# Performance work log

Hardware: AMD Instinct MI355X
Metric: run time of the kernel (lower is better)

## Reference

```python
import jax, jax.numpy as jnp
import numpy as np

B, T, DIM, NH = 2, 2048, 1024, 16
HD = DIM // NH  # 64


def setup_inputs() -> dict:
    key = jax.random.key(0)
    ks = jax.random.split(key, 5)
    x = jax.random.normal(ks[0], (B, T, DIM), dtype=jnp.float32)
    # realistic RoPE tables (any float tables work; use true rotary angles)
    inv_freq = 1.0 / (10000.0 ** (jnp.arange(0, HD, 2, dtype=jnp.float32) / HD))  # [HD/2]
    ang = jnp.arange(T, dtype=jnp.float32)[:, None] * inv_freq[None, :]           # [T, HD/2]
    ang = jnp.repeat(ang, 2, axis=-1)                                             # [T, HD] interleaved pairs
    sin = jnp.sin(ang)[None, None]  # [1,1,T,HD]
    cos = jnp.cos(ang)[None, None]
    W_qkv = jax.random.normal(ks[1], (DIM, 3 * DIM), dtype=jnp.float32) * (DIM ** -0.5)
    W_proj = jax.random.normal(ks[2], (DIM, DIM), dtype=jnp.float32) * (DIM ** -0.5)
    return {"x": x, "sin": sin, "cos": cos, "W_qkv": W_qkv, "W_proj": W_proj}


def _rope(x, sin, cos):
    # x: [B,H,T,D]; sin/cos: [1,1,T,D]
    x1, x2 = x[..., ::2], x[..., 1::2]
    xr = jnp.stack((-x2, x1), axis=-1).reshape(x.shape)  # interleave (-x2, x1)
    return x * cos + xr * sin


def reference(x, sin, cos, W_qkv, W_proj):
    Bx, Tx, C = x.shape
    nh, hd = NH, C // NH
    qkv = x @ W_qkv                                   # [B,T,3C]
    q, k, v = jnp.split(qkv, 3, axis=-1)
    to_bhtd = lambda t: t.reshape(Bx, Tx, nh, hd).transpose(0, 2, 1, 3)
    q, k, v = to_bhtd(q), to_bhtd(k), to_bhtd(v)      # [B,H,T,D]
    q = _rope(q, sin[:, :, :Tx], cos[:, :, :Tx])
    k = _rope(k, sin[:, :, :Tx], cos[:, :, :Tx])
    scale = 1.0 / jnp.sqrt(jnp.asarray(hd, dtype=x.dtype))
    scores = jnp.einsum('bhqd,bhkd->bhqk', q, k) * scale
    causal = jnp.tril(jnp.ones((Tx, Tx), dtype=bool))
    scores = jnp.where(causal, scores, jnp.finfo(scores.dtype).min)
    attn = jax.nn.softmax(scores, axis=-1)
    y = jnp.einsum('bhqk,bhkd->bhqd', attn, v)        # [B,H,T,D]
    y = y.transpose(0, 2, 1, 3).reshape(Bx, Tx, C)
    return y @ W_proj
```

## Files before the change

### kernel.cpp

```cpp
#include <hip/hip_runtime.h>


typedef float  f32x4  __attribute__((ext_vector_type(4)));
typedef __bf16 bf16x8 __attribute__((ext_vector_type(8)));
typedef short  short8 __attribute__((ext_vector_type(8)));

#define Bb   2
#define Tt   2048
#define DIMc 1024
#define NHh  16
#define HDd  64

__device__ __forceinline__ short f2bf(float f) {
    unsigned u = __builtin_bit_cast(unsigned, f);
    u += 0x7fffu + ((u >> 16) & 1u);
    return (short)(u >> 16);
}

__device__ __forceinline__ f32x4 mfma16(short8 a, short8 b, f32x4 c) {
    return __builtin_amdgcn_mfma_f32_16x16x32_bf16(
        __builtin_bit_cast(bf16x8, a), __builtin_bit_cast(bf16x8, b), c, 0, 0, 0);
}

__device__ __forceinline__ void gl_lds16(const void* g, void* l) {
    __builtin_amdgcn_global_load_lds(
        (const __attribute__((address_space(1))) unsigned int*)g,
        (__attribute__((address_space(3))) unsigned int*)l, 16, 0, 0);
}

__global__ __launch_bounds__(256) void convX(const float* __restrict__ X,
                                             short* __restrict__ Xb)
{
    size_t i = ((size_t)blockIdx.x * 256 + threadIdx.x) * 8;
    float4 a = *(const float4*)(X + i);
    float4 b = *(const float4*)(X + i + 4);
    short8 s;
    s[0] = f2bf(a.x); s[1] = f2bf(a.y); s[2] = f2bf(a.z); s[3] = f2bf(a.w);
    s[4] = f2bf(b.x); s[5] = f2bf(b.y); s[6] = f2bf(b.z); s[7] = f2bf(b.w);
    *(short8*)(Xb + i) = s;
}

__global__ __launch_bounds__(256) void convT(const float* __restrict__ W,
                                             short* __restrict__ Wt, int N)
{
    __shared__ float L[64][65];
    const int kb = blockIdx.x * 64, nb = blockIdx.y * 64;
    const int tid = threadIdx.x;
#pragma unroll
    for (int it = 0; it < 4; it++) {
        int kk = it * 16 + (tid >> 4), c = (tid & 15) * 4;
        float4 v = *(const float4*)(W + (size_t)(kb + kk) * N + nb + c);
        L[c + 0][kk] = v.x; L[c + 1][kk] = v.y;
        L[c + 2][kk] = v.z; L[c + 3][kk] = v.w;
    }
    __syncthreads();
#pragma unroll
    for (int it = 0; it < 2; it++) {
        int n = it * 32 + (tid >> 3), ks = (tid & 7) * 8;
        short8 s;
#pragma unroll
        for (int j = 0; j < 8; j++) s[j] = f2bf(L[n][ks + j]);
        *(short8*)(Wt + (size_t)(nb + n) * 1024 + kb + ks) = s;
    }
}

__global__ __launch_bounds__(256) void qkv_rope(
    const short* __restrict__ A, const short* __restrict__ Bt,
    const float* __restrict__ Sn, const float* __restrict__ Cs,
    short* __restrict__ Qo, short* __restrict__ Ko, short* __restrict__ Vt)
{
    __shared__ __align__(16) short As[128][32];
    __shared__ __align__(16) short Bs[128][32];
    const int bm = blockIdx.x, bn = blockIdx.y;
    const int tid = threadIdx.x;
    const int wv = tid >> 6, lane = tid & 63, g = lane >> 4, l16 = lane & 15;
    const int wr = wv >> 1, wc = wv & 1;

    f32x4 acc[4][4];
#pragma unroll
    for (int i = 0; i < 4; i++)
#pragma unroll
        for (int j = 0; j < 4; j++) acc[i][j] = (f32x4){0.f, 0.f, 0.f, 0.f};

    const int rA = tid >> 2, cA = (tid & 3) << 3;
    for (int k0 = 0; k0 < 1024; k0 += 32) {
#pragma unroll
        for (int i = 0; i < 2; i++)
            gl_lds16(A + (size_t)(bm * 128 + i * 64 + rA) * 1024 + k0 + cA,
                     &As[i * 64 + rA][cA]);
#pragma unroll
        for (int i = 0; i < 2; i++)
            gl_lds16(Bt + (size_t)(bn * 128 + i * 64 + rA) * 1024 + k0 + cA,
                     &Bs[i * 64 + rA][cA]);
        __syncthreads();
        short8 af[4], bfr[4];
#pragma unroll
        for (int mt = 0; mt < 4; mt++) af[mt]  = *(const short8*)&As[wr * 64 + mt * 16 + l16][g * 8];
#pragma unroll
        for (int nt = 0; nt < 4; nt++) bfr[nt] = *(const short8*)&Bs[wc * 64 + nt * 16 + l16][g * 8];
#pragma unroll
        for (int mt = 0; mt < 4; mt++)
#pragma unroll
            for (int nt = 0; nt < 4; nt++) acc[mt][nt] = mfma16(af[mt], bfr[nt], acc[mt][nt]);
        __syncthreads();
    }

#pragma unroll
    for (int mt = 0; mt < 4; mt++)
#pragma unroll
        for (int nt = 0; nt < 4; nt++)
#pragma unroll
            for (int r = 0; r < 4; r++) {
                int m = bm * 128 + wr * 64 + mt * 16 + g * 4 + r;
                int n = bn * 128 + wc * 64 + nt * 16 + l16;
                float val = acc[mt][nt][r];
                float partner = __shfl_xor(val, 1, 64);
                int b = m >> 11, t = m & 2047;
                int sec = n >> 10, nn = n & 1023;
                int h = nn >> 6, d = nn & 63;
                if (sec == 2) {
                    Vt[(((size_t)(b * 16 + h) * 64 + d) << 11) + t] = f2bf(val);
                } else {
                    float sv = Sn[t * 64 + d], cv = Cs[t * 64 + d];
                    float ro = (d & 1) ? fmaf(val, cv, partner * sv)
                                       : fmaf(val, cv, -partner * sv);
                    short* dst = (sec == 0) ? Qo : Ko;
                    dst[(((size_t)(b * 16 + h) << 11) + t) * 64 + d] = f2bf(ro);
                }
            }
}

__global__ __launch_bounds__(256, 4) void attn(
    const short* __restrict__ Q, const short* __restrict__ K,
    const short* __restrict__ V, short* __restrict__ Y)
{
    __shared__ __align__(16) short Ks[2][64][64];
    __shared__ __align__(16) short Vs[2][64][64];
    __shared__ __align__(16) short Pl[4][16][64];

    const int id = blockIdx.y * gridDim.x + blockIdx.x;
    const int bh = id >> 5;
    const int qi = ((id & 31) + ((id >> 8) << 3)) & 31;
    const int tid = threadIdx.x, wv = tid >> 6, lane = tid & 63;
    const int g = lane >> 4, l16 = lane & 15;
    const int q0w = qi * 64 + wv * 16;
    const short* Qb = Q + (size_t)bh * Tt * 64;
    const short* Kb = K + (size_t)bh * Tt * 64;
    const short* Vb = V + (size_t)bh * 64 * Tt;

    const int rj = lane >> 3, cc = lane & 7, gc = cc ^ rj;

    auto stage = [&](int s, int buf) {
        int k0s = s * 64;
#pragma unroll
        for (int j = 0; j < 2; j++) {
            int row = wv * 16 + j * 8 + rj;
            gl_lds16(Kb + (size_t)(k0s + row) * 64 + gc * 8, &Ks[buf][row][cc << 3]);
        }
#pragma unroll
        for (int j = 0; j < 2; j++) {
            int row = wv * 16 + j * 8 + rj;
            gl_lds16(Vb + (size_t)row * Tt + k0s + gc * 8, &Vs[buf][row][cc << 3]);
        }
    };

    short8 qf[2];
#pragma unroll
    for (int ss = 0; ss < 2; ss++)
        qf[ss] = *(const short8*)(Qb + (size_t)(q0w + l16) * 64 + ss * 32 + g * 8);

    f32x4 o[4];
#pragma unroll
    for (int nt = 0; nt < 4; nt++) o[nt] = (f32x4){0.f, 0.f, 0.f, 0.f};
    float lsum[4] = {0.f, 0.f, 0.f, 0.f};

    const int nsteps = qi + 1;
    const int sw = l16 & 7;

    stage(0, 0);
    __syncthreads();

    for (int s = 0; s < nsteps; ++s) {
        if (s + 1 < nsteps) stage(s + 1, (s + 1) & 1);
        const int kb = s & 1, k0 = s * 64;

        f32x4 S[4];
#pragma unroll
        for (int t = 0; t < 4; t++) {
            S[t] = (f32x4){0.f, 0.f, 0.f, 0.f};
#pragma unroll
            for (int ss = 0; ss < 2; ss++) {
                short8 kf = *(const short8*)&Ks[kb][t * 16 + l16][((ss * 4 + g) ^ sw) << 3];
                S[t] = mfma16(qf[ss], kf, S[t]);
            }
        }

        float p[4][4];
        if (s < nsteps - 1) {
#pragma unroll
            for (int t = 0; t < 4; t++)
#pragma unroll
                for (int r = 0; r < 4; r++)
                    p[t][r] = __expf(fmaf(S[t][r], 0.125f, -10.f));
        } else {
#pragma unroll
            for (int t = 0; t < 4; t++)
#pragma unroll
                for (int r = 0; r < 4; r++) {
                    int key = k0 + t * 16 + l16, qq = q0w + g * 4 + r;
                    p[t][r] = (key <= qq) ? __expf(fmaf(S[t][r], 0.125f, -10.f)) : 0.f;
                }
        }
#pragma unroll
        for (int r = 0; r < 4; r++)
            lsum[r] += (p[0][r] + p[1][r]) + (p[2][r] + p[3][r]);

#pragma unroll
        for (int t = 0; t < 4; t++)
#pragma unroll
            for (int r = 0; r < 4; r++) {
                int row = g * 4 + r, c = t * 16 + l16;
                Pl[wv][row][(((c >> 3) ^ (row & 7)) << 3) | (c & 7)] = f2bf(p[t][r]);
            }
        asm volatile("" ::: "memory");
        short8 pf[2];
#pragma unroll
        for (int ks = 0; ks < 2; ks++)
            pf[ks] = *(const short8*)&Pl[wv][l16][((ks * 4 + g) ^ sw) << 3];
#pragma unroll
        for (int nt = 0; nt < 4; nt++)
#pragma unroll
            for (int ks = 0; ks < 2; ks++) {
                short8 vf = *(const short8*)&Vs[kb][nt * 16 + l16][((ks * 4 + g) ^ sw) << 3];
                o[nt] = mfma16(pf[ks], vf, o[nt]);
            }
        __syncthreads();
    }

    float inv[4];
#pragma unroll
    for (int r = 0; r < 4; r++) {
        float t = lsum[r];
        t += __shfl_xor(t, 1, 64);
        t += __shfl_xor(t, 2, 64);
        t += __shfl_xor(t, 4, 64);
        t += __shfl_xor(t, 8, 64);
        inv[r] = 1.0f / t;
    }
    const int b = bh >> 4, h = bh & 15;
#pragma unroll
    for (int nt = 0; nt < 4; nt++)
#pragma unroll
        for (int r = 0; r < 4; r++) {
            int qq = q0w + g * 4 + r, d = nt * 16 + l16;
            Y[((size_t)(b * Tt + qq)) * DIMc + h * 64 + d] = f2bf(o[nt][r] * inv[r]);
        }
}

__global__ __launch_bounds__(256) void proj(
    const short* __restrict__ A, const short* __restrict__ Bt, float* __restrict__ O)
{
    __shared__ __align__(16) short As[128][32];
    __shared__ __align__(16) short Bs[128][32];
    const int bm = blockIdx.x, bn = blockIdx.y;
    const int tid = threadIdx.x;
    const int wv = tid >> 6, lane = tid & 63, g = lane >> 4, l16 = lane & 15;
    const int wr = wv >> 1, wc = wv & 1;

    f32x4 acc[4][4];
#pragma unroll
    for (int i = 0; i < 4; i++)
#pragma unroll
        for (int j = 0; j < 4; j++) acc[i][j] = (f32x4){0.f, 0.f, 0.f, 0.f};

    const int rA = tid >> 2, cA = (tid & 3) << 3;
    for (int k0 = 0; k0 < 1024; k0 += 32) {
#pragma unroll
        for (int i = 0; i < 2; i++)
            gl_lds16(A + (size_t)(bm * 128 + i * 64 + rA) * 1024 + k0 + cA,
                     &As[i * 64 + rA][cA]);
#pragma unroll
        for (int i = 0; i < 2; i++)
            gl_lds16(Bt + (size_t)(bn * 128 + i * 64 + rA) * 1024 + k0 + cA,
                     &Bs[i * 64 + rA][cA]);
        __syncthreads();
        short8 af[4], bfr[4];
#pragma unroll
        for (int mt = 0; mt < 4; mt++) af[mt]  = *(const short8*)&As[wr * 64 + mt * 16 + l16][g * 8];
#pragma unroll
        for (int nt = 0; nt < 4; nt++) bfr[nt] = *(const short8*)&Bs[wc * 64 + nt * 16 + l16][g * 8];
#pragma unroll
        for (int mt = 0; mt < 4; mt++)
#pragma unroll
            for (int nt = 0; nt < 4; nt++) acc[mt][nt] = mfma16(af[mt], bfr[nt], acc[mt][nt]);
        __syncthreads();
    }

#pragma unroll
    for (int mt = 0; mt < 4; mt++)
#pragma unroll
        for (int nt = 0; nt < 4; nt++)
#pragma unroll
            for (int r = 0; r < 4; r++) {
                int m = bm * 128 + wr * 64 + mt * 16 + g * 4 + r;
                int n = bn * 128 + wc * 64 + nt * 16 + l16;
                O[(size_t)m * 1024 + n] = acc[mt][nt][r];
            }
}

extern "C" void kernel_launch(void* const* d_in, const int* in_sizes, int n_in,
                              void* d_out, int out_size, void* d_ws, size_t ws_size,
                              hipStream_t stream)
{
    const float* x     = (const float*)d_in[0];
    const float* sn    = (const float*)d_in[1];
    const float* cs    = (const float*)d_in[2];
    const float* wqkv  = (const float*)d_in[3];
    const float* wproj = (const float*)d_in[4];
    float* out = (float*)d_out;

    char* ws = (char*)d_ws;
    const size_t MB = 1024 * 1024;
    short* q   = (short*)(ws);
    short* k   = (short*)(ws + 8  * MB);
    short* vt  = (short*)(ws + 16 * MB);
    short* y   = (short*)(ws + 24 * MB);
    short* xb  = (short*)(ws + 32 * MB);
    short* wqt = (short*)(ws + 40 * MB);
    short* wpt = (short*)(ws + 46 * MB);

    convX<<<2048, 256, 0, stream>>>(x, xb);
    convT<<<dim3(16, 48), 256, 0, stream>>>(wqkv, wqt, 3072);
    convT<<<dim3(16, 16), 256, 0, stream>>>(wproj, wpt, 1024);
    qkv_rope<<<dim3(32, 24), 256, 0, stream>>>(xb, wqt, sn, cs, q, k, vt);
    attn<<<dim3(Tt / 64, Bb * NHh), 256, 0, stream>>>(q, k, vt, y);
    proj<<<dim3(32, 8), 256, 0, stream>>>(y, wpt, out);
}
```

Baseline: 204.1 us.

## Fuse prep kernels, use BK=64 swizzled GEMM tiles, pair causal attention tiles

Merges the three conversion kernels into one launch. Both GEMMs move to a K-tile of 64 with XOR-swizzled LDS, which halves the number of barriers per K. Attention now gives each block two query tiles (qi and 31-qi) so the causal work per block is even, and the grid is halved. The row-sum of P is computed with an MFMA against a vector of ones instead of shuffles, the exp moves to exp2f, and P is cast to bf16 by truncation. Truncating P and relying on a fixed max offset instead of a running max may change accuracy slightly.

```diff
diff --git a/kernel.cpp b/kernel.cpp
--- a/kernel.cpp
+++ b/kernel.cpp
@@ -16,6 +16,9 @@
     u += 0x7fffu + ((u >> 16) & 1u);
     return (short)(u >> 16);
 }
+__device__ __forceinline__ short f2bf_t(float f) {
+    return (short)(__builtin_bit_cast(unsigned, f) >> 16);
+}
 
 __device__ __forceinline__ f32x4 mfma16(short8 a, short8 b, f32x4 c) {
     return __builtin_amdgcn_mfma_f32_16x16x32_bf16(
@@ -28,24 +31,27 @@
         (__attribute__((address_space(3))) unsigned int*)l, 16, 0, 0);
 }
 
-__global__ __launch_bounds__(256) void convX(const float* __restrict__ X,
-                                             short* __restrict__ Xb)
-{
-    size_t i = ((size_t)blockIdx.x * 256 + threadIdx.x) * 8;
-    float4 a = *(const float4*)(X + i);
-    float4 b = *(const float4*)(X + i + 4);
-    short8 s;
-    s[0] = f2bf(a.x); s[1] = f2bf(a.y); s[2] = f2bf(a.z); s[3] = f2bf(a.w);
-    s[4] = f2bf(b.x); s[5] = f2bf(b.y); s[6] = f2bf(b.z); s[7] = f2bf(b.w);
-    *(short8*)(Xb + i) = s;
-}
-
-__global__ __launch_bounds__(256) void convT(const float* __restrict__ W,
-                                             short* __restrict__ Wt, int N)
+__global__ __launch_bounds__(256) void prep(
+    const float* __restrict__ X,  short* __restrict__ Xb,
+    const float* __restrict__ Wq, short* __restrict__ Wqt,
+    const float* __restrict__ Wp, short* __restrict__ Wpt)
 {
     __shared__ float L[64][65];
-    const int kb = blockIdx.x * 64, nb = blockIdx.y * 64;
-    const int tid = threadIdx.x;
+    const int id = blockIdx.x, tid = threadIdx.x;
+    if (id < 2048) {
+        size_t i = ((size_t)id * 256 + tid) * 8;
+        float4 a = *(const float4*)(X + i);
+        float4 b = *(const float4*)(X + i + 4);
+        short8 s;
+        s[0] = f2bf(a.x); s[1] = f2bf(a.y); s[2] = f2bf(a.z); s[3] = f2bf(a.w);
+        s[4] = f2bf(b.x); s[5] = f2bf(b.y); s[6] = f2bf(b.z); s[7] = f2bf(b.w);
+        *(short8*)(Xb + i) = s;
+        return;
+    }
+    const float* W; short* Wt; int N, id2;
+    if (id < 2816) { W = Wq; Wt = Wqt; N = 3072; id2 = id - 2048; }
+    else           { W = Wp; Wt = Wpt; N = 1024; id2 = id - 2816; }
+    const int kb = (id2 & 15) * 64, nb = (id2 >> 4) * 64;
 #pragma unroll
     for (int it = 0; it < 4; it++) {
         int kk = it * 16 + (tid >> 4), c = (tid & 15) * 4;
@@ -64,13 +70,50 @@
     }
 }
 
+#define GEMM_BK64_LOOP(Aptr, Bptr, lda, ldb)                                      \
+    const int rj = lane >> 3, cc = lane & 7, gc8 = (cc ^ rj) * 8;                 \
+    const int sw = l16 & 7;                                                       \
+    for (int k0 = 0; k0 < 1024; k0 += 64) {                                       \
+        _Pragma("unroll")                                                         \
+        for (int i = 0; i < 4; i++) {                                             \
+            int row = i * 32 + wv * 8 + rj;                                       \
+            gl_lds16(Aptr + (size_t)(bm * 128 + row) * lda + k0 + gc8,            \
+                     &As[row][cc * 8]);                                           \
+        }                                                                         \
+        _Pragma("unroll")                                                         \
+        for (int i = 0; i < 4; i++) {                                             \
+            int row = i * 32 + wv * 8 + rj;                                       \
+            gl_lds16(Bptr + (size_t)(bn * 128 + row) * ldb + k0 + gc8,            \
+                     &Bs[row][cc * 8]);                                           \
+        }                                                                         \
+        __syncthreads();                                                          \
+        _Pragma("unroll")                                                         \
+        for (int kk8 = 0; kk8 < 2; kk8++) {                                       \
+            short8 af[4], bfr[4];                                                 \
+            _Pragma("unroll")                                                     \
+            for (int mt = 0; mt < 4; mt++)                                        \
+                af[mt] = *(const short8*)&As[wr * 64 + mt * 16 + l16]             \
+                                           [((kk8 * 4 + g) ^ sw) * 8];            \
+            _Pragma("unroll")                                                     \
+            for (int nt = 0; nt < 4; nt++)                                        \
+                bfr[nt] = *(const short8*)&Bs[wc * 64 + nt * 16 + l16]            \
+                                            [((kk8 * 4 + g) ^ sw) * 8];           \
+            _Pragma("unroll")                                                     \
+            for (int mt = 0; mt < 4; mt++)                                        \
+                _Pragma("unroll")                                                 \
+                for (int nt = 0; nt < 4; nt++)                                    \
+                    acc[mt][nt] = mfma16(af[mt], bfr[nt], acc[mt][nt]);           \
+        }                                                                         \
+        __syncthreads();                                                          \
+    }
+
 __global__ __launch_bounds__(256) void qkv_rope(
     const short* __restrict__ A, const short* __restrict__ Bt,
     const float* __restrict__ Sn, const float* __restrict__ Cs,
     short* __restrict__ Qo, short* __restrict__ Ko, short* __restrict__ Vt)
 {
-    __shared__ __align__(16) short As[128][32];
-    __shared__ __align__(16) short Bs[128][32];
+    __shared__ __align__(16) short As[128][64];
+    __shared__ __align__(16) short Bs[128][64];
     const int bm = blockIdx.x, bn = blockIdx.y;
     const int tid = threadIdx.x;
     const int wv = tid >> 6, lane = tid & 63, g = lane >> 4, l16 = lane & 15;
@@ -82,28 +125,7 @@
 #pragma unroll
         for (int j = 0; j < 4; j++) acc[i][j] = (f32x4){0.f, 0.f, 0.f, 0.f};
 
-    const int rA = tid >> 2, cA = (tid & 3) << 3;
-    for (int k0 = 0; k0 < 1024; k0 += 32) {
-#pragma unroll
-        for (int i = 0; i < 2; i++)
-            gl_lds16(A + (size_t)(bm * 128 + i * 64 + rA) * 1024 + k0 + cA,
-                     &As[i * 64 + rA][cA]);
-#pragma unroll
-        for (int i = 0; i < 2; i++)
-            gl_lds16(Bt + (size_t)(bn * 128 + i * 64 + rA) * 1024 + k0 + cA,
-                     &Bs[i * 64 + rA][cA]);
-        __syncthreads();
-        short8 af[4], bfr[4];
-#pragma unroll
-        for (int mt = 0; mt < 4; mt++) af[mt]  = *(const short8*)&As[wr * 64 + mt * 16 + l16][g * 8];
-#pragma unroll
-        for (int nt = 0; nt < 4; nt++) bfr[nt] = *(const short8*)&Bs[wc * 64 + nt * 16 + l16][g * 8];
-#pragma unroll
-        for (int mt = 0; mt < 4; mt++)
-#pragma unroll
-            for (int nt = 0; nt < 4; nt++) acc[mt][nt] = mfma16(af[mt], bfr[nt], acc[mt][nt]);
-        __syncthreads();
-    }
+    GEMM_BK64_LOOP(A, Bt, 1024, 1024)
 
 #pragma unroll
     for (int mt = 0; mt < 4; mt++)
@@ -138,17 +160,20 @@
     __shared__ __align__(16) short Vs[2][64][64];
     __shared__ __align__(16) short Pl[4][16][64];
 
-    const int id = blockIdx.y * gridDim.x + blockIdx.x;
-    const int bh = id >> 5;
-    const int qi = ((id & 31) + ((id >> 8) << 3)) & 31;
+    const int bh = blockIdx.y;
     const int tid = threadIdx.x, wv = tid >> 6, lane = tid & 63;
     const int g = lane >> 4, l16 = lane & 15;
-    const int q0w = qi * 64 + wv * 16;
     const short* Qb = Q + (size_t)bh * Tt * 64;
     const short* Kb = K + (size_t)bh * Tt * 64;
     const short* Vb = V + (size_t)bh * 64 * Tt;
+    const int b = bh >> 4, h = bh & 15;
 
     const int rj = lane >> 3, cc = lane & 7, gc = cc ^ rj;
+    const int sw = l16 & 7;
+
+    short8 ones;
+#pragma unroll
+    for (int j = 0; j < 8; j++) ones[j] = (short)0x3F80;
 
     auto stage = [&](int s, int buf) {
         int k0s = s * 64;
@@ -164,104 +189,99 @@
         }
     };
 
-    short8 qf[2];
-#pragma unroll
-    for (int ss = 0; ss < 2; ss++)
-        qf[ss] = *(const short8*)(Qb + (size_t)(q0w + l16) * 64 + ss * 32 + g * 8);
-
-    f32x4 o[4];
-#pragma unroll
-    for (int nt = 0; nt < 4; nt++) o[nt] = (f32x4){0.f, 0.f, 0.f, 0.f};
-    float lsum[4] = {0.f, 0.f, 0.f, 0.f};
-
-    const int nsteps = qi + 1;
-    const int sw = l16 & 7;
-
-    stage(0, 0);
-    __syncthreads();
-
-    for (int s = 0; s < nsteps; ++s) {
-        if (s + 1 < nsteps) stage(s + 1, (s + 1) & 1);
-        const int kb = s & 1, k0 = s * 64;
-
-        f32x4 S[4];
-#pragma unroll
-        for (int t = 0; t < 4; t++) {
-            S[t] = (f32x4){0.f, 0.f, 0.f, 0.f};
-#pragma unroll
-            for (int ss = 0; ss < 2; ss++) {
-                short8 kf = *(const short8*)&Ks[kb][t * 16 + l16][((ss * 4 + g) ^ sw) << 3];
-                S[t] = mfma16(qf[ss], kf, S[t]);
-            }
+    for (int pass = 0; pass < 2; pass++) {
+        const int qi = pass ? (31 - blockIdx.x) : blockIdx.x;
+        const int q0w = qi * 64 + wv * 16;
+        const int nsteps = qi + 1;
+
+        short8 qf[2];
+#pragma unroll
+        for (int ss = 0; ss < 2; ss++)
+            qf[ss] = *(const short8*)(Qb + (size_t)(q0w + l16) * 64 + ss * 32 + g * 8);
+
+        f32x4 o[4], lacc = (f32x4){0.f, 0.f, 0.f, 0.f};
+#pragma unroll
+        for (int nt = 0; nt < 4; nt++) o[nt] = (f32x4){0.f, 0.f, 0.f, 0.f};
+
+        __syncthreads();
+        stage(0, 0);
+        __syncthreads();
+
+        for (int s = 0; s < nsteps; ++s) {
+            if (s + 1 < nsteps) stage(s + 1, (s + 1) & 1);
+            const int kb = s & 1, k0 = s * 64;
+
+            f32x4 S[4];
+#pragma unroll
+            for (int t = 0; t < 4; t++) {
+                S[t] = (f32x4){0.f, 0.f, 0.f, 0.f};
+#pragma unroll
+                for (int ss = 0; ss < 2; ss++) {
+                    short8 kf = *(const short8*)&Ks[kb][t * 16 + l16][((ss * 4 + g) ^ sw) << 3];
+                    S[t] = mfma16(qf[ss], kf, S[t]);
+                }
+            }
+
+            float p[4][4];
+            if (s < nsteps - 1) {
+#pragma unroll
+                for (int t = 0; t < 4; t++)
+#pragma unroll
+                    for (int r = 0; r < 4; r++)
+                        p[t][r] = exp2f(fmaf(S[t][r], 0.18033688f, -14.4269504f));
+            } else {
+#pragma unroll
+                for (int t = 0; t < 4; t++)
+#pragma unroll
+                    for (int r = 0; r < 4; r++) {
+                        int key = k0 + t * 16 + l16, qq = q0w + g * 4 + r;
+                        p[t][r] = (key <= qq)
+                                  ? exp2f(fmaf(S[t][r], 0.18033688f, -14.4269504f)) : 0.f;
+                    }
+            }
+
+#pragma unroll
+            for (int t = 0; t < 4; t++)
+#pragma unroll
+                for (int r = 0; r < 4; r++) {
+                    int row = g * 4 + r, c = t * 16 + l16;
+                    Pl[wv][row][(((c >> 3) ^ (row & 7)) << 3) | (c & 7)] = f2bf_t(p[t][r]);
+                }
+            asm volatile("" ::: "memory");
+            short8 pf[2];
+#pragma unroll
+            for (int ks = 0; ks < 2; ks++)
+                pf[ks] = *(const short8*)&Pl[wv][l16][((ks * 4 + g) ^ sw) << 3];
+#pragma unroll
+            for (int ks = 0; ks < 2; ks++) {
+                lacc = mfma16(pf[ks], ones, lacc);
+#pragma unroll
+                for (int nt = 0; nt < 4; nt++) {
+                    short8 vf = *(const short8*)&Vs[kb][nt * 16 + l16][((ks * 4 + g) ^ sw) << 3];
+                    o[nt] = mfma16(pf[ks], vf, o[nt]);
+                }
+            }
+            __syncthreads();
         }
 
-        float p[4][4];
-        if (s < nsteps - 1) {
-#pragma unroll
-            for (int t = 0; t < 4; t++)
-#pragma unroll
-                for (int r = 0; r < 4; r++)
-                    p[t][r] = __expf(fmaf(S[t][r], 0.125f, -10.f));
-        } else {
-#pragma unroll
-            for (int t = 0; t < 4; t++)
-#pragma unroll
-                for (int r = 0; r < 4; r++) {
-                    int key = k0 + t * 16 + l16, qq = q0w + g * 4 + r;
-                    p[t][r] = (key <= qq) ? __expf(fmaf(S[t][r], 0.125f, -10.f)) : 0.f;
-                }
-        }
-#pragma unroll
-        for (int r = 0; r < 4; r++)
-            lsum[r] += (p[0][r] + p[1][r]) + (p[2][r] + p[3][r]);
-
-#pragma unroll
-        for (int t = 0; t < 4; t++)
+        float inv[4];
+#pragma unroll
+        for (int r = 0; r < 4; r++) inv[r] = 1.0f / lacc[r];
+#pragma unroll
+        for (int nt = 0; nt < 4; nt++)
 #pragma unroll
             for (int r = 0; r < 4; r++) {
-                int row = g * 4 + r, c = t * 16 + l16;
-                Pl[wv][row][(((c >> 3) ^ (row & 7)) << 3) | (c & 7)] = f2bf(p[t][r]);
-            }
-        asm volatile("" ::: "memory");
-        short8 pf[2];
-#pragma unroll
-        for (int ks = 0; ks < 2; ks++)
-            pf[ks] = *(const short8*)&Pl[wv][l16][((ks * 4 + g) ^ sw) << 3];
-#pragma unroll
-        for (int nt = 0; nt < 4; nt++)
-#pragma unroll
-            for (int ks = 0; ks < 2; ks++) {
-                short8 vf = *(const short8*)&Vs[kb][nt * 16 + l16][((ks * 4 + g) ^ sw) << 3];
-                o[nt] = mfma16(pf[ks], vf, o[nt]);
-            }
-        __syncthreads();
-    }
-
-    float inv[4];
-#pragma unroll
-    for (int r = 0; r < 4; r++) {
-        float t = lsum[r];
-        t += __shfl_xor(t, 1, 64);
-        t += __shfl_xor(t, 2, 64);
-        t += __shfl_xor(t, 4, 64);
-        t += __shfl_xor(t, 8, 64);
-        inv[r] = 1.0f / t;
-    }
-    const int b = bh >> 4, h = bh & 15;
-#pragma unroll
-    for (int nt = 0; nt < 4; nt++)
-#pragma unroll
-        for (int r = 0; r < 4; r++) {
-            int qq = q0w + g * 4 + r, d = nt * 16 + l16;
-            Y[((size_t)(b * Tt + qq)) * DIMc + h * 64 + d] = f2bf(o[nt][r] * inv[r]);
-        }
+                int qq = q0w + g * 4 + r, d = nt * 16 + l16;
+                Y[((size_t)(b * Tt + qq)) * DIMc + h * 64 + d] = f2bf(o[nt][r] * inv[r]);
+            }
+    }
 }
 
 __global__ __launch_bounds__(256) void proj(
     const short* __restrict__ A, const short* __restrict__ Bt, float* __restrict__ O)
 {
-    __shared__ __align__(16) short As[128][32];
-    __shared__ __align__(16) short Bs[128][32];
+    __shared__ __align__(16) short As[128][64];
+    __shared__ __align__(16) short Bs[128][64];
     const int bm = blockIdx.x, bn = blockIdx.y;
     const int tid = threadIdx.x;
     const int wv = tid >> 6, lane = tid & 63, g = lane >> 4, l16 = lane & 15;
@@ -273,28 +293,7 @@
 #pragma unroll
         for (int j = 0; j < 4; j++) acc[i][j] = (f32x4){0.f, 0.f, 0.f, 0.f};
 
-    const int rA = tid >> 2, cA = (tid & 3) << 3;
-    for (int k0 = 0; k0 < 1024; k0 += 32) {
-#pragma unroll
-        for (int i = 0; i < 2; i++)
-            gl_lds16(A + (size_t)(bm * 128 + i * 64 + rA) * 1024 + k0 + cA,
-                     &As[i * 64 + rA][cA]);
-#pragma unroll
-        for (int i = 0; i < 2; i++)
-            gl_lds16(Bt + (size_t)(bn * 128 + i * 64 + rA) * 1024 + k0 + cA,
-                     &Bs[i * 64 + rA][cA]);
-        __syncthreads();
-        short8 af[4], bfr[4];
-#pragma unroll
-        for (int mt = 0; mt < 4; mt++) af[mt]  = *(const short8*)&As[wr * 64 + mt * 16 + l16][g * 8];
-#pragma unroll
-        for (int nt = 0; nt < 4; nt++) bfr[nt] = *(const short8*)&Bs[wc * 64 + nt * 16 + l16][g * 8];
-#pragma unroll
-        for (int mt = 0; mt < 4; mt++)
-#pragma unroll
-            for (int nt = 0; nt < 4; nt++) acc[mt][nt] = mfma16(af[mt], bfr[nt], acc[mt][nt]);
-        __syncthreads();
-    }
+    GEMM_BK64_LOOP(A, Bt, 1024, 1024)
 
 #pragma unroll
     for (int mt = 0; mt < 4; mt++)
@@ -329,10 +328,8 @@
     short* wqt = (short*)(ws + 40 * MB);
     short* wpt = (short*)(ws + 46 * MB);
 
-    convX<<<2048, 256, 0, stream>>>(x, xb);
-    convT<<<dim3(16, 48), 256, 0, stream>>>(wqkv, wqt, 3072);
-    convT<<<dim3(16, 16), 256, 0, stream>>>(wproj, wpt, 1024);
+    prep<<<3072, 256, 0, stream>>>(x, xb, wqkv, wqt, wproj, wpt);
     qkv_rope<<<dim3(32, 24), 256, 0, stream>>>(xb, wqt, sn, cs, q, k, vt);
-    attn<<<dim3(Tt / 64, Bb * NHh), 256, 0, stream>>>(q, k, vt, y);
+    attn<<<dim3(16, Bb * NHh), 256, 0, stream>>>(q, k, vt, y);
     proj<<<dim3(32, 8), 256, 0, stream>>>(y, wpt, out);
 }
```

Result: slower. 220.1 us (+7.8%).
